# Optimization experiments

Measured on AMD Instinct MI355X. Metric: run time of the kernel, lower is better.

The kernel has to match this reference:

```python
import jax, jax.numpy as jnp
import numpy as np

S = 4          # num_residual_streams
B = 4          # batch
T = 4096       # seq_len
D = 1024       # dim
SINKHORN_ITERS = 20
EPS = 1e-05


def setup_inputs() -> dict:
    key = jax.random.key(0)
    k1, k2 = jax.random.split(key)
    residuals = jax.random.normal(k1, (B * S, T, D), dtype=jnp.float32)
    rmsnorm_weight = jnp.ones((D,), dtype=jnp.float32)
    # H_pre: -8 everywhere except layer_index % S = 0 -> 0.0
    H_pre_logits = jnp.full((S,), -8.0, dtype=jnp.float32).at[0].set(0.0)
    H_post_logits = jnp.zeros((S,), dtype=jnp.float32)
    # H_res: -8 off-diagonal, 0 on diagonal, plus alpha_init * noise
    H_res = (jnp.full((S, S), -8.0, dtype=jnp.float32) + 8.0 * jnp.eye(S, dtype=jnp.float32)
             + 0.01 * jax.random.normal(k2, (S, S), dtype=jnp.float32))
    return dict(residuals=residuals, rmsnorm_weight=rmsnorm_weight,
                H_pre_logits=H_pre_logits, H_post_logits=H_post_logits, H_res=H_res)


def _sinkhorn_knopp(M, num_iters, eps):
    # alternating row / column normalization to a doubly-stochastic matrix
    for _ in range(num_iters):
        M = M / (M.sum(axis=1, keepdims=True) + eps)
        M = M / (M.sum(axis=0, keepdims=True) + eps)
    return M


def reference(residuals, rmsnorm_weight, H_pre_logits, H_post_logits, H_res):
    s = H_pre_logits.shape[0]
    bs, t, d = residuals.shape
    b = bs // s
    # rearrange '(b s) t d -> (b t) s d'
    x = residuals.reshape(b, s, t, d).transpose(0, 2, 1, 3).reshape(b * t, s, d)
    # stream_aggregate with h_pre = sigmoid(H_pre_logits)
    h_pre = jax.nn.sigmoid(H_pre_logits)
    x_agg = jnp.einsum('nsd,s->nd', x, h_pre)
    # rmsnorm
    rms = jnp.sqrt(jnp.mean(x_agg * x_agg, axis=-1, keepdims=True) + EPS)
    x_norm = (x_agg / rms) * rmsnorm_weight
    # identity branch on the aggregated single-stream view
    branch_out = x_norm  # [(b t), d]
    # stream_distribute with h_post = 2 * sigmoid(H_post_logits)
    h_post = 2.0 * jax.nn.sigmoid(H_post_logits)
    y_dist = branch_out[:, None, :] * h_post[None, :, None]  # [(b t), s, d]
    # stream_mix with sinkhorn-normalized exp(H_res)
    M = _sinkhorn_knopp(jnp.exp(H_res), SINKHORN_ITERS, EPS)
    mixed = jnp.einsum('sr,nrd->nsd', M, y_dist)
    out = x + mixed
    # rearrange '(b t) s d -> (b s) t d'
    out = out.reshape(b, t, s, d).transpose(0, 2, 1, 3).reshape(b * s, t, d)
    return out
```

## Files before the change

kernel.cpp:

```cpp
#include <hip/hip_runtime.h>


#define S_ 4
#define T_ 4096
#define D_ 1024
#define NITER_ 20
#define EPSF_ 1e-5f

typedef float f32x4 __attribute__((ext_vector_type(4)));

__device__ float g_coef[8];

__global__ void hyperconn_coeff(const float* __restrict__ hpre_l,
                                const float* __restrict__ hpost_l,
                                const float* __restrict__ hres)
{
    if (threadIdx.x != 0) return;

    float M[S_][S_];
    #pragma unroll
    for (int i = 0; i < S_; ++i)
        #pragma unroll
        for (int j = 0; j < S_; ++j)
            M[i][j] = __expf(hres[i * S_ + j]);

    for (int it = 0; it < NITER_; ++it) {
        #pragma unroll
        for (int i = 0; i < S_; ++i) {
            float inv = 1.0f / (M[i][0] + M[i][1] + M[i][2] + M[i][3] + EPSF_);
            M[i][0] *= inv; M[i][1] *= inv; M[i][2] *= inv; M[i][3] *= inv;
        }
        #pragma unroll
        for (int j = 0; j < S_; ++j) {
            float inv = 1.0f / (M[0][j] + M[1][j] + M[2][j] + M[3][j] + EPSF_);
            M[0][j] *= inv; M[1][j] *= inv; M[2][j] *= inv; M[3][j] *= inv;
        }
    }

    #pragma unroll
    for (int s = 0; s < S_; ++s) {
        g_coef[s] = 1.0f / (1.0f + __expf(-hpre_l[s]));
        float c = 0.0f;
        #pragma unroll
        for (int r = 0; r < S_; ++r)
            c += M[s][r] * (2.0f / (1.0f + __expf(-hpost_l[r])));
        g_coef[S_ + s] = c;
    }
}

__global__ __launch_bounds__(256) void hyperconn_main(
    const float* __restrict__ res,
    const float* __restrict__ w,
    float* __restrict__ out)
{
    const int n   = blockIdx.x;
    const int b   = n >> 12;
    const int t   = n & (T_ - 1);
    const int tid = threadIdx.x;

    __shared__ float s_part[4];

    const float h0 = g_coef[0], h1 = g_coef[1], h2 = g_coef[2], h3 = g_coef[3];
    const float c0 = g_coef[4], c1 = g_coef[5], c2 = g_coef[6], c3 = g_coef[7];

    const f32x4* res4 = reinterpret_cast<const f32x4*>(res);
    const f32x4* w4   = reinterpret_cast<const f32x4*>(w);
    f32x4*       out4 = reinterpret_cast<f32x4*>(out);

    const int    D4      = D_ / 4;
    const size_t rowbase = (size_t)(b * S_) * T_ + t;
    const size_t sstride = (size_t)T_ * D4;

    const size_t base = rowbase * D4 + tid;
    f32x4 r[S_];
    #pragma unroll
    for (int s = 0; s < S_; ++s)
        r[s] = __builtin_nontemporal_load(&res4[base + (size_t)s * sstride]);

    f32x4 agg = h0 * r[0] + h1 * r[1] + h2 * r[2] + h3 * r[3];

    float ssq = agg.x*agg.x + agg.y*agg.y + agg.z*agg.z + agg.w*agg.w;
    #pragma unroll
    for (int off = 32; off >= 1; off >>= 1)
        ssq += __shfl_down(ssq, off, 64);
    const int lane = tid & 63;
    const int wv   = tid >> 6;
    if (lane == 0) s_part[wv] = ssq;
    __syncthreads();
    const float tot     = s_part[0] + s_part[1] + s_part[2] + s_part[3];
    const float inv_rms = rsqrtf(tot * (1.0f / (float)D_) + EPSF_);

    const f32x4 wt  = w4[tid];
    const f32x4 nrm = agg * inv_rms * wt;

    const float cs[S_] = {c0, c1, c2, c3};
    #pragma unroll
    for (int s = 0; s < S_; ++s) {
        f32x4 o = r[s] + nrm * cs[s];
        __builtin_nontemporal_store(o, &out4[base + (size_t)s * sstride]);
    }
}

extern "C" void kernel_launch(void* const* d_in, const int* in_sizes, int n_in,
                              void* d_out, int out_size, void* d_ws, size_t ws_size,
                              hipStream_t stream) {
    const float* res     = (const float*)d_in[0];
    const float* weight  = (const float*)d_in[1];
    const float* hpre_l  = (const float*)d_in[2];
    const float* hpost_l = (const float*)d_in[3];
    const float* hres    = (const float*)d_in[4];
    float*       out     = (float*)d_out;

    hyperconn_coeff<<<1, 64, 0, stream>>>(hpre_l, hpost_l, hres);

    const int n_rows = in_sizes[0] / (S_ * D_);
    hyperconn_main<<<n_rows, 256, 0, stream>>>(res, weight, out);
}
```

Before: 456.3 us.

## Process one row per wavefront with grid-stride loop and shuffle-only reduction

Each wavefront now handles a whole row (1024 elements, 4 float4 per lane per stream), so the RMS reduction uses only xor-shuffles and needs neither shared memory nor a block barrier. The grid is fixed at 1024 persistent blocks that stride over rows, and the weight vector is loaded once per wave instead of once per row. Nontemporal load and store hints are dropped in favour of plain accesses. Each lane holds 16 float4 of residuals, which raises register pressure, and a fixed grid may leave fewer loads in flight than one block per row did.

```diff
diff --git a/kernel.cpp b/kernel.cpp
--- a/kernel.cpp
+++ b/kernel.cpp
@@ -48,56 +48,66 @@
     }
 }
 
-__global__ __launch_bounds__(256) void hyperconn_main(
+__global__ __launch_bounds__(256, 4) void hyperconn_main(
     const float* __restrict__ res,
     const float* __restrict__ w,
-    float* __restrict__ out)
+    float* __restrict__ out,
+    const int n_rows)
 {
-    const int n   = blockIdx.x;
-    const int b   = n >> 12;
-    const int t   = n & (T_ - 1);
-    const int tid = threadIdx.x;
-
-    __shared__ float s_part[4];
+    const int lane = threadIdx.x & 63;
+    const int gw   = (int)((blockIdx.x * blockDim.x + threadIdx.x) >> 6);
+    const int nw   = (int)((gridDim.x * blockDim.x) >> 6);
 
     const float h0 = g_coef[0], h1 = g_coef[1], h2 = g_coef[2], h3 = g_coef[3];
-    const float c0 = g_coef[4], c1 = g_coef[5], c2 = g_coef[6], c3 = g_coef[7];
+    const float cs0 = g_coef[4], cs1 = g_coef[5], cs2 = g_coef[6], cs3 = g_coef[7];
+    const float cs[S_] = {cs0, cs1, cs2, cs3};
 
     const f32x4* res4 = reinterpret_cast<const f32x4*>(res);
     const f32x4* w4   = reinterpret_cast<const f32x4*>(w);
     f32x4*       out4 = reinterpret_cast<f32x4*>(out);
 
-    const int    D4      = D_ / 4;
-    const size_t rowbase = (size_t)(b * S_) * T_ + t;
-    const size_t sstride = (size_t)T_ * D4;
+    const size_t sstride = (size_t)T_ * (D_ / 4);
 
-    const size_t base = rowbase * D4 + tid;
-    f32x4 r[S_];
+    f32x4 wt[4];
     #pragma unroll
-    for (int s = 0; s < S_; ++s)
-        r[s] = __builtin_nontemporal_load(&res4[base + (size_t)s * sstride]);
+    for (int k = 0; k < 4; ++k)
+        wt[k] = w4[(k << 6) + lane];
 
-    f32x4 agg = h0 * r[0] + h1 * r[1] + h2 * r[2] + h3 * r[3];
+    for (int n = gw; n < n_rows; n += nw) {
+        const int b = n >> 12;
+        const int t = n & (T_ - 1);
+        const size_t rb = ((size_t)(b * S_) * T_ + t) * (D_ / 4) + lane;
 
-    float ssq = agg.x*agg.x + agg.y*agg.y + agg.z*agg.z + agg.w*agg.w;
-    #pragma unroll
-    for (int off = 32; off >= 1; off >>= 1)
-        ssq += __shfl_down(ssq, off, 64);
-    const int lane = tid & 63;
-    const int wv   = tid >> 6;
-    if (lane == 0) s_part[wv] = ssq;
-    __syncthreads();
-    const float tot     = s_part[0] + s_part[1] + s_part[2] + s_part[3];
-    const float inv_rms = rsqrtf(tot * (1.0f / (float)D_) + EPSF_);
+        f32x4 r[S_][4];
+        #pragma unroll
+        for (int s = 0; s < S_; ++s)
+            #pragma unroll
+            for (int k = 0; k < 4; ++k)
+                r[s][k] = res4[rb + (size_t)s * sstride + (k << 6)];
 
-    const f32x4 wt  = w4[tid];
-    const f32x4 nrm = agg * inv_rms * wt;
+        f32x4 agg[4];
+        #pragma unroll
+        for (int k = 0; k < 4; ++k)
+            agg[k] = h0 * r[0][k] + h1 * r[1][k] + h2 * r[2][k] + h3 * r[3][k];
 
-    const float cs[S_] = {c0, c1, c2, c3};
-    #pragma unroll
-    for (int s = 0; s < S_; ++s) {
-        f32x4 o = r[s] + nrm * cs[s];
-        __builtin_nontemporal_store(o, &out4[base + (size_t)s * sstride]);
+        float ssq = 0.0f;
+        #pragma unroll
+        for (int k = 0; k < 4; ++k)
+            ssq += agg[k].x*agg[k].x + agg[k].y*agg[k].y
+                 + agg[k].z*agg[k].z + agg[k].w*agg[k].w;
+        #pragma unroll
+        for (int off = 1; off <= 32; off <<= 1)
+            ssq += __shfl_xor(ssq, off, 64);
+
+        const float inv_rms = rsqrtf(ssq * (1.0f / (float)D_) + EPSF_);
+
+        #pragma unroll
+        for (int k = 0; k < 4; ++k) {
+            const f32x4 nrm = agg[k] * inv_rms * wt[k];
+            #pragma unroll
+            for (int s = 0; s < S_; ++s)
+                out4[rb + (size_t)s * sstride + (k << 6)] = r[s][k] + nrm * cs[s];
+        }
     }
 }
 
@@ -114,5 +124,5 @@
     hyperconn_coeff<<<1, 64, 0, stream>>>(hpre_l, hpost_l, hres);
 
     const int n_rows = in_sizes[0] / (S_ * D_);
-    hyperconn_main<<<n_rows, 256, 0, stream>>>(res, weight, out);
+    hyperconn_main<<<1024, 256, 0, stream>>>(res, weight, out, n_rows);
 }
```

New measurement: 454.4 us. No clear change (-0.4%).
